# Performance work log

Hardware: AMD Instinct MI355X
Metric: run time of the kernel (lower is better)

## Reference

```python
import jax, jax.numpy as jnp
import numpy as np

B = 16384
C = 512          # mean candidate count per sample
T = B * C        # total flat logits length (static)


def _seg_ce(logits, counts, gt, valid, B):
    """Segmented cross-entropy over variable-length candidate sets.
    logits: [T] flat concatenated logits; counts: [B] segment lengths (sum == T);
    gt: [B] target index within each segment; valid: [B] bool mask.
    Returns (mean loss over valid samples, n_correct, n_valid)."""
    Ttot = logits.shape[0]
    offsets = jnp.cumsum(counts) - counts                       # [B] start of each segment
    seg = jnp.repeat(jnp.arange(B), counts, total_repeat_length=Ttot)  # [T] segment ids
    segmax = jax.ops.segment_max(logits, seg, num_segments=B)   # [B]
    ex = jnp.exp(logits - segmax[seg])
    Z = jax.ops.segment_sum(ex, seg, num_segments=B)            # [B]
    lse = jnp.log(Z) + segmax                                   # [B] logsumexp per segment
    # target logit: clamp position for safety; invalid rows are masked out anyway
    pos = offsets + jnp.clip(gt, 0, jnp.maximum(counts - 1, 0))
    ce = lse - logits[pos]                                      # [B]
    in_range = (gt >= 0) & (gt < counts)
    vmask = (counts > 0) & in_range & valid
    n_valid = vmask.sum()
    loss = jnp.where(vmask, ce, 0.0).sum() / jnp.maximum(n_valid, 1)
    # argmax within each segment (first occurrence, matching torch.argmax)
    local = jnp.arange(Ttot) - offsets[seg]
    is_max = logits == segmax[seg]
    arg = jax.ops.segment_min(jnp.where(is_max, local, Ttot), seg, num_segments=B)
    n_correct = (vmask & (arg == gt)).sum()
    return loss, n_correct, n_valid


def setup_inputs() -> dict:
    key = jax.random.key(0)
    ks = jax.random.split(key, 8)
    # counts alternate C+32 / C-32 so sum == B*C exactly (static T)
    counts = jnp.where(jnp.arange(B) % 2 == 0, C + 32, C - 32).astype(jnp.int32)
    sys_logits = jax.random.normal(ks[0], (T,), dtype=jnp.float32)
    bar_logits = jax.random.normal(ks[1], (T,), dtype=jnp.float32)
    gt_system_idx = jax.random.randint(ks[2], (B,), 0, C - 32).astype(jnp.int32)
    gt_bar_in_sys = jax.random.randint(ks[3], (B,), 0, C - 32).astype(jnp.int32)
    note_positions = jax.random.uniform(ks[4], (B,), dtype=jnp.float32)
    gt_note_position = jax.random.uniform(ks[5], (B,), dtype=jnp.float32)
    gt_valid = jax.random.bernoulli(ks[6], 0.97, (B,))
    return {
        'sys_logits': sys_logits, 'sys_counts': counts,
        'bar_logits': bar_logits, 'bar_counts': counts,
        'note_positions': note_positions,
        'gt_system_idx': gt_system_idx, 'gt_bar_in_sys': gt_bar_in_sys,
        'gt_note_position': gt_note_position, 'gt_valid': gt_valid,
        'log_var_sys': jnp.zeros((), jnp.float32),
        'log_var_bar': jnp.zeros((), jnp.float32),
        'log_var_note': jnp.zeros((), jnp.float32),
    }


def reference(sys_logits, sys_counts, bar_logits, bar_counts, note_positions,
              gt_system_idx, gt_bar_in_sys, gt_note_position, gt_valid,
              log_var_sys, log_var_bar, log_var_note):
    Bn = gt_system_idx.shape[0]
    sys_loss, sys_correct, n_valid = _seg_ce(sys_logits, sys_counts, gt_system_idx, gt_valid, Bn)
    bar_loss, bar_correct, n_valid_bar = _seg_ce(bar_logits, bar_counts, gt_bar_in_sys, gt_valid, Bn)
    # note position MSE over valid samples (bar_valid == gt_valid here)
    m = gt_valid
    nsel = m.sum()
    sq = jnp.where(m, (note_positions - gt_note_position) ** 2, 0.0)
    note_loss = jnp.where(nsel > 0, sq.sum() / jnp.maximum(nsel, 1), 0.0)
    prec_sys = jnp.exp(-log_var_sys)
    prec_bar = jnp.exp(-log_var_bar)
    prec_note = jnp.exp(-log_var_note)
    loss = (0.5 * prec_sys * sys_loss + 0.5 * log_var_sys
            + 0.5 * prec_bar * bar_loss + 0.5 * log_var_bar
            + 0.5 * prec_note * note_loss + 0.5 * log_var_note)
    sys_acc = sys_correct / jnp.maximum(n_valid, 1)
    bar_acc = bar_correct / jnp.maximum(n_valid_bar, 1)
    return (loss, sys_loss, bar_loss, note_loss, sys_acc, bar_acc,
            prec_sys, prec_bar, prec_note)
```

## Files before the change

### kernel.cpp

```cpp
#include <hip/hip_runtime.h>
#include <math.h>


#define SCAN_BLOCKS 64
#define OFFS_BASE 512

__device__ __forceinline__ bool is_valid(const void* gv, int flag, int i) {
  if (flag == 0) return ((const int*)gv)[i] != 0;
  if (flag == 1) return ((const unsigned char*)gv)[i] != 0;
  return ((const float*)gv)[i] != 0.0f;
}

__global__ __launch_bounds__(256)
void uwl_scan_partial(const int* __restrict__ c_sys, const int* __restrict__ c_bar,
                      int B, int* __restrict__ part) {
  const int blk = blockIdx.x;
  const int chunk = (B + SCAN_BLOCKS - 1) / SCAN_BLOCKS;
  const int start = blk * chunk;
  const int end = (start + chunk < B) ? start + chunk : B;
  int ss = 0, sb = 0;
  for (int i = start + threadIdx.x; i < end; i += 256) {
    ss += c_sys[i];
    sb += c_bar[i];
  }
#pragma unroll
  for (int d = 1; d < 64; d <<= 1) {
    ss += __shfl_xor(ss, d, 64);
    sb += __shfl_xor(sb, d, 64);
  }
  __shared__ int l1[4], l2[4];
  const int wid = threadIdx.x >> 6;
  if ((threadIdx.x & 63) == 0) { l1[wid] = ss; l2[wid] = sb; }
  __syncthreads();
  if (threadIdx.x == 0) {
    part[blk] = l1[0] + l1[1] + l1[2] + l1[3];
    part[SCAN_BLOCKS + blk] = l2[0] + l2[1] + l2[2] + l2[3];
  }
}

__global__ void uwl_scan_mid(const void* __restrict__ gv, int B, int* ws, int* part) {
  const int lane = threadIdx.x;
  int a = part[lane], b = part[SCAN_BLOCKS + lane];
  int ia = a, ib = b;
#pragma unroll
  for (int d = 1; d < 64; d <<= 1) {
    const int va = __shfl_up(ia, d, 64);
    const int vb = __shfl_up(ib, d, 64);
    if (lane >= d) { ia += va; ib += vb; }
  }
  part[lane] = ia - a;
  part[SCAN_BLOCKS + lane] = ib - b;
  if (lane >= 1 && lane <= 8) ws[lane * 16] = 0;
  if (lane == 0) {
    const unsigned int* w = (const unsigned int*)gv;
    int nw = B / 4; if (nw > 64) nw = 64; if (nw < 1) nw = 1;
    bool all01 = true, allf = true;
    for (int i = 0; i < nw; ++i) {
      const unsigned int x = w[i];
      if (x > 1u) all01 = false;
      if (x != 0u && x != 0x3F800000u) allf = false;
    }
    ws[0] = all01 ? 0 : (allf ? 2 : 1);
  }
}

__global__ __launch_bounds__(256)
void uwl_scan_final(const int* __restrict__ c_sys, const int* __restrict__ c_bar,
                    int B, int* __restrict__ ws, const int* __restrict__ part) {
  const int blk = blockIdx.x;
  const int chunk = (B + SCAN_BLOCKS - 1) / SCAN_BLOCKS;
  const int start = blk * chunk;
  const int end = (start + chunk < B) ? start + chunk : B;
  const int lane = threadIdx.x & 63;
  const int wid = threadIdx.x >> 6;
  __shared__ int ws1[4], ws2[4];
  int carry1 = part[blk], carry2 = part[SCAN_BLOCKS + blk];
  for (int base = start; base < end; base += 256) {
    const int idx = base + threadIdx.x;
    const bool ok = idx < end;
    const int x1 = ok ? c_sys[idx] : 0;
    const int x2 = ok ? c_bar[idx] : 0;
    int o1 = x1, o2 = x2;
#pragma unroll
    for (int d = 1; d < 64; d <<= 1) {
      const int v1 = __shfl_up(o1, d, 64);
      const int v2 = __shfl_up(o2, d, 64);
      if (lane >= d) { o1 += v1; o2 += v2; }
    }
    if (lane == 63) { ws1[wid] = o1; ws2[wid] = o2; }
    __syncthreads();
    int w1 = 0, w2 = 0;
    for (int w = 0; w < wid; ++w) { w1 += ws1[w]; w2 += ws2[w]; }
    if (ok) {
      ws[OFFS_BASE + idx]     = carry1 + w1 + o1 - x1;
      ws[OFFS_BASE + B + idx] = carry2 + w2 + o2 - x2;
    }
    carry1 += ws1[0] + ws1[1] + ws1[2] + ws1[3];
    carry2 += ws2[0] + ws2[1] + ws2[2] + ws2[3];
    __syncthreads();
  }
}

__global__ __launch_bounds__(256)
void uwl_ce_kernel(const float* __restrict__ sys_lg, const float* __restrict__ bar_lg,
                   const int* __restrict__ c_sys, const int* __restrict__ c_bar,
                   const int* __restrict__ gt_sys, const int* __restrict__ gt_bar,
                   const void* __restrict__ gv, int B, int* wsI, float* wsF) {
  const int wave = (blockIdx.x * blockDim.x + threadIdx.x) >> 6;
  const int lane = threadIdx.x & 63;
  if (wave >= 2 * B) return;
  const bool is_sys = wave < B;
  const int b = is_sys ? wave : wave - B;
  const float* lg = is_sys ? sys_lg : bar_lg;
  const int count = (is_sys ? c_sys : c_bar)[b];
  const int off_i = wsI[OFFS_BASE + (is_sys ? 0 : B) + b];
  const long long off = off_i;
  const int gt = (is_sys ? gt_sys : gt_bar)[b];

  float m = -INFINITY;
  int mi = 0x7fffffff;
  float vals[12];
  const bool regpath = (count <= 768) && ((off_i & 3) == 0);
  if (regpath) {
    const float4* p = (const float4*)(lg + off);
#pragma unroll
    for (int k = 0; k < 3; ++k) {
      const int e = (k << 8) + (lane << 2);
      if (e + 3 < count) {
        const float4 v = p[(k << 6) + lane];
        vals[4 * k] = v.x; vals[4 * k + 1] = v.y;
        vals[4 * k + 2] = v.z; vals[4 * k + 3] = v.w;
      } else {
#pragma unroll
        for (int j = 0; j < 4; ++j) {
          const int i = e + j;
          vals[4 * k + j] = (i < count) ? lg[off + i] : -INFINITY;
        }
      }
    }
#pragma unroll
    for (int k = 0; k < 3; ++k)
#pragma unroll
      for (int j = 0; j < 4; ++j) {
        const float v = vals[4 * k + j];
        if (v > m) { m = v; mi = (k << 8) + (lane << 2) + j; }
      }
  } else {
    for (int i = lane; i < count; i += 64) {
      const float v = lg[off + i];
      if (v > m) { m = v; mi = i; }
    }
  }
#pragma unroll
  for (int d = 1; d < 64; d <<= 1) {
    const float om = __shfl_xor(m, d, 64);
    const int omi = __shfl_xor(mi, d, 64);
    if (om > m || (om == m && omi < mi)) { m = om; mi = omi; }
  }
  float s = 0.f;
  if (regpath) {
#pragma unroll
    for (int k = 0; k < 12; ++k) s += __expf(vals[k] - m);
  } else {
    for (int i = lane; i < count; i += 64) s += __expf(lg[off + i] - m);
  }
#pragma unroll
  for (int d = 1; d < 64; d <<= 1) s += __shfl_xor(s, d, 64);

  if (lane == 0) {
    float ce = 0.f;
    int code = 0;
    if (count > 0) {
      const int flag = wsI[0];
      const bool in_range = (gt >= 0) && (gt < count);
      if (in_range && is_valid(gv, flag, b)) {
        const float tl = lg[off + gt];
        ce = __logf(s) + m - tl;
        code = 1 | ((mi == gt) ? 2 : 0);
      }
    }
    wsF[OFFS_BASE + 2 * B + wave] = ce;
    wsI[OFFS_BASE + 4 * B + wave] = code;
  }
}

__global__ __launch_bounds__(256)
void uwl_reduce_kernel(const float* __restrict__ npos, const float* __restrict__ gnp,
                       const void* __restrict__ gv, int B, int* wsI, float* wsF) {
  const float* ceArr = wsF + OFFS_BASE + 2 * B;
  const int* codeArr = wsI + OFFS_BASE + 4 * B;
  float ces = 0.f, ceb = 0.f;
  int nvs = 0, cs = 0, nvb = 0, cb = 0;
  const int stride = gridDim.x * blockDim.x;
  for (int i = blockIdx.x * blockDim.x + threadIdx.x; i < 2 * B; i += stride) {
    const float ce = ceArr[i];
    const int code = codeArr[i];
    if (i < B) { ces += ce; nvs += code & 1; cs += code >> 1; }
    else       { ceb += ce; nvb += code & 1; cb += code >> 1; }
  }
  const int flag = wsI[0];
  float sq = 0.f; int cnt = 0;
  for (int i = blockIdx.x * blockDim.x + threadIdx.x; i < B; i += stride) {
    if (is_valid(gv, flag, i)) {
      const float d = npos[i] - gnp[i];
      sq += d * d; cnt += 1;
    }
  }
#pragma unroll
  for (int d = 1; d < 64; d <<= 1) {
    ces += __shfl_xor(ces, d, 64);
    ceb += __shfl_xor(ceb, d, 64);
    nvs += __shfl_xor(nvs, d, 64);
    cs  += __shfl_xor(cs,  d, 64);
    nvb += __shfl_xor(nvb, d, 64);
    cb  += __shfl_xor(cb,  d, 64);
    sq  += __shfl_xor(sq,  d, 64);
    cnt += __shfl_xor(cnt, d, 64);
  }
  if ((threadIdx.x & 63) == 0) {
    atomicAdd(&wsI[16], nvs);
    atomicAdd(&wsI[32], cs);
    atomicAdd(&wsF[48], ces);
    atomicAdd(&wsI[64], nvb);
    atomicAdd(&wsI[80], cb);
    atomicAdd(&wsF[96], ceb);
    atomicAdd(&wsI[112], cnt);
    atomicAdd(&wsF[128], sq);
  }
}

__global__ void uwl_final_kernel(const float* __restrict__ lvs_p, const float* __restrict__ lvb_p,
                                 const float* __restrict__ lvn_p,
                                 const int* wsI, const float* wsF, float* __restrict__ out) {
  if (threadIdx.x != 0 || blockIdx.x != 0) return;
  const int nvs = wsI[16], cs = wsI[32], nvb = wsI[64], cb = wsI[80], nn = wsI[112];
  const float sys_loss = wsF[48] / (float)(nvs > 1 ? nvs : 1);
  const float bar_loss = wsF[96] / (float)(nvb > 1 ? nvb : 1);
  const float note_loss = (nn > 0) ? wsF[128] / (float)nn : 0.f;
  const float lvs = lvs_p[0], lvb = lvb_p[0], lvn = lvn_p[0];
  const float ps = expf(-lvs), pb = expf(-lvb), pn = expf(-lvn);
  const float loss = 0.5f * (ps * sys_loss + lvs + pb * bar_loss + lvb + pn * note_loss + lvn);
  out[0] = loss;
  out[1] = sys_loss;
  out[2] = bar_loss;
  out[3] = note_loss;
  out[4] = (float)cs / (float)(nvs > 1 ? nvs : 1);
  out[5] = (float)cb / (float)(nvb > 1 ? nvb : 1);
  out[6] = ps;
  out[7] = pb;
  out[8] = pn;
}

extern "C" void kernel_launch(void* const* d_in, const int* in_sizes, int n_in,
                              void* d_out, int out_size, void* d_ws, size_t ws_size,
                              hipStream_t stream) {
  const float* sys_lg = (const float*)d_in[0];
  const int*   c_sys  = (const int*)d_in[1];
  const float* bar_lg = (const float*)d_in[2];
  const int*   c_bar  = (const int*)d_in[3];
  const float* npos   = (const float*)d_in[4];
  const int*   gt_sys = (const int*)d_in[5];
  const int*   gt_bar = (const int*)d_in[6];
  const float* gnp    = (const float*)d_in[7];
  const void*  gv     = d_in[8];
  const float* lvs    = (const float*)d_in[9];
  const float* lvb    = (const float*)d_in[10];
  const float* lvn    = (const float*)d_in[11];
  const int B = in_sizes[1];

  int*   wsI = (int*)d_ws;
  float* wsF = (float*)d_ws;
  int*   part = wsI + 256;

  uwl_scan_partial<<<SCAN_BLOCKS, 256, 0, stream>>>(c_sys, c_bar, B, part);
  uwl_scan_mid<<<1, 64, 0, stream>>>(gv, B, wsI, part);
  uwl_scan_final<<<SCAN_BLOCKS, 256, 0, stream>>>(c_sys, c_bar, B, wsI, part);

  const int nwaves = 2 * B;
  const long long nthreads = (long long)nwaves * 64;
  const int nblocks = (int)((nthreads + 255) / 256);
  uwl_ce_kernel<<<nblocks, 256, 0, stream>>>(sys_lg, bar_lg, c_sys, c_bar,
                                             gt_sys, gt_bar, gv, B, wsI, wsF);

  uwl_reduce_kernel<<<64, 256, 0, stream>>>(npos, gnp, gv, B, wsI, wsF);

  uwl_final_kernel<<<1, 64, 0, stream>>>(lvs, lvb, lvn, wsI, wsF, (float*)d_out);
}
```

Before: 143.1 us.

## Merge scan stages, precompute per-segment descriptors, and fuse final reduction

Removes the single-block mid-scan kernel by having each final-scan block reduce the partial sums of the blocks before it. The scan now writes one int4 descriptor per segment (offset, count, gt, validity), so the CE kernel does a single load instead of several scattered ones. The target logit is taken from registers via a shuffle rather than a dependent global load. The final scalar kernel is folded into the reduce kernel with a last-block-done atomic counter. Launch count drops from six to four, at the cost of extra workspace traffic for the wider descriptors and a threadfence-based completion protocol.

```diff
diff --git a/kernel.cpp b/kernel.cpp
--- a/kernel.cpp
+++ b/kernel.cpp
@@ -1,9 +1,8 @@
 #include <hip/hip_runtime.h>
 #include <math.h>
 
-
 #define SCAN_BLOCKS 64
-#define OFFS_BASE 512
+#define DESC_BASE 512
 
 __device__ __forceinline__ bool is_valid(const void* gv, int flag, int i) {
   if (flag == 0) return ((const int*)gv)[i] != 0;
@@ -13,7 +12,7 @@
 
 __global__ __launch_bounds__(256)
 void uwl_scan_partial(const int* __restrict__ c_sys, const int* __restrict__ c_bar,
-                      int B, int* __restrict__ part) {
+                      const void* __restrict__ gv, int B, int* __restrict__ ws) {
   const int blk = blockIdx.x;
   const int chunk = (B + SCAN_BLOCKS - 1) / SCAN_BLOCKS;
   const int start = blk * chunk;
@@ -33,48 +32,50 @@
   if ((threadIdx.x & 63) == 0) { l1[wid] = ss; l2[wid] = sb; }
   __syncthreads();
   if (threadIdx.x == 0) {
-    part[blk] = l1[0] + l1[1] + l1[2] + l1[3];
-    part[SCAN_BLOCKS + blk] = l2[0] + l2[1] + l2[2] + l2[3];
-  }
-}
-
-__global__ void uwl_scan_mid(const void* __restrict__ gv, int B, int* ws, int* part) {
-  const int lane = threadIdx.x;
-  int a = part[lane], b = part[SCAN_BLOCKS + lane];
-  int ia = a, ib = b;
-#pragma unroll
-  for (int d = 1; d < 64; d <<= 1) {
-    const int va = __shfl_up(ia, d, 64);
-    const int vb = __shfl_up(ib, d, 64);
-    if (lane >= d) { ia += va; ib += vb; }
-  }
-  part[lane] = ia - a;
-  part[SCAN_BLOCKS + lane] = ib - b;
-  if (lane >= 1 && lane <= 8) ws[lane * 16] = 0;
-  if (lane == 0) {
-    const unsigned int* w = (const unsigned int*)gv;
-    int nw = B / 4; if (nw > 64) nw = 64; if (nw < 1) nw = 1;
-    bool all01 = true, allf = true;
-    for (int i = 0; i < nw; ++i) {
-      const unsigned int x = w[i];
-      if (x > 1u) all01 = false;
-      if (x != 0u && x != 0x3F800000u) allf = false;
-    }
-    ws[0] = all01 ? 0 : (allf ? 2 : 1);
-  }
-}
-
-__global__ __launch_bounds__(256)
-void uwl_scan_final(const int* __restrict__ c_sys, const int* __restrict__ c_bar,
-                    int B, int* __restrict__ ws, const int* __restrict__ part) {
+    ws[256 + blk] = l1[0] + l1[1] + l1[2] + l1[3];
+    ws[256 + SCAN_BLOCKS + blk] = l2[0] + l2[1] + l2[2] + l2[3];
+  }
+  if (blk == 0) {
+    if (threadIdx.x >= 1 && threadIdx.x <= 8) ws[threadIdx.x * 16] = 0;
+    if (threadIdx.x == 9) ws[144] = 0;
+    if (threadIdx.x == 10) {
+      const unsigned int* w = (const unsigned int*)gv;
+      int nw = B / 4; if (nw > 64) nw = 64; if (nw < 1) nw = 1;
+      bool all01 = true, allf = true;
+      for (int i = 0; i < nw; ++i) {
+        const unsigned int x = w[i];
+        if (x > 1u) all01 = false;
+        if (x != 0u && x != 0x3F800000u) allf = false;
+      }
+      ws[0] = all01 ? 0 : (allf ? 2 : 1);
+    }
+  }
+}
+
+__global__ __launch_bounds__(256)
+void uwl_scan_desc(const int* __restrict__ c_sys, const int* __restrict__ c_bar,
+                   const int* __restrict__ gt_sys, const int* __restrict__ gt_bar,
+                   const void* __restrict__ gv, int B, int* __restrict__ ws) {
+  const int* part = ws + 256;
+  const int flag = ws[0];
   const int blk = blockIdx.x;
+  const int lane = threadIdx.x & 63;
+  const int wid = threadIdx.x >> 6;
+  __shared__ int baseS, baseB;
+  __shared__ int ws1[4], ws2[4];
+  if (threadIdx.x < 128) {
+    int p = (lane < blk) ? part[(wid ? SCAN_BLOCKS : 0) + lane] : 0;
+#pragma unroll
+    for (int d = 1; d < 64; d <<= 1) p += __shfl_xor(p, d, 64);
+    if (lane == 0) { if (wid) baseB = p; else baseS = p; }
+  }
+  __syncthreads();
+  int carry1 = baseS, carry2 = baseB;
   const int chunk = (B + SCAN_BLOCKS - 1) / SCAN_BLOCKS;
   const int start = blk * chunk;
   const int end = (start + chunk < B) ? start + chunk : B;
-  const int lane = threadIdx.x & 63;
-  const int wid = threadIdx.x >> 6;
-  __shared__ int ws1[4], ws2[4];
-  int carry1 = part[blk], carry2 = part[SCAN_BLOCKS + blk];
+  int4* descS = (int4*)(ws + DESC_BASE);
+  int4* descB = descS + B;
   for (int base = start; base < end; base += 256) {
     const int idx = base + threadIdx.x;
     const bool ok = idx < end;
@@ -92,8 +93,12 @@
     int w1 = 0, w2 = 0;
     for (int w = 0; w < wid; ++w) { w1 += ws1[w]; w2 += ws2[w]; }
     if (ok) {
-      ws[OFFS_BASE + idx]     = carry1 + w1 + o1 - x1;
-      ws[OFFS_BASE + B + idx] = carry2 + w2 + o2 - x2;
+      const int g1 = gt_sys[idx], g2 = gt_bar[idx];
+      const bool v = is_valid(gv, flag, idx);
+      descS[idx] = make_int4(carry1 + w1 + o1 - x1, x1, g1,
+                             (x1 > 0 && g1 >= 0 && g1 < x1 && v) ? 1 : 0);
+      descB[idx] = make_int4(carry2 + w2 + o2 - x2, x2, g2,
+                             (x2 > 0 && g2 >= 0 && g2 < x2 && v) ? 1 : 0);
     }
     carry1 += ws1[0] + ws1[1] + ws1[2] + ws1[3];
     carry2 += ws2[0] + ws2[1] + ws2[2] + ws2[3];
@@ -103,19 +108,14 @@
 
 __global__ __launch_bounds__(256)
 void uwl_ce_kernel(const float* __restrict__ sys_lg, const float* __restrict__ bar_lg,
-                   const int* __restrict__ c_sys, const int* __restrict__ c_bar,
-                   const int* __restrict__ gt_sys, const int* __restrict__ gt_bar,
-                   const void* __restrict__ gv, int B, int* wsI, float* wsF) {
+                   int B, int* __restrict__ wsI, float* __restrict__ wsF) {
   const int wave = (blockIdx.x * blockDim.x + threadIdx.x) >> 6;
   const int lane = threadIdx.x & 63;
   if (wave >= 2 * B) return;
-  const bool is_sys = wave < B;
-  const int b = is_sys ? wave : wave - B;
-  const float* lg = is_sys ? sys_lg : bar_lg;
-  const int count = (is_sys ? c_sys : c_bar)[b];
-  const int off_i = wsI[OFFS_BASE + (is_sys ? 0 : B) + b];
+  const int4 d4 = ((const int4*)(wsI + DESC_BASE))[wave];
+  const float* lg = (wave < B) ? sys_lg : bar_lg;
+  const int off_i = d4.x, count = d4.y, gt = d4.z, vld = d4.w;
   const long long off = off_i;
-  const int gt = (is_sys ? gt_sys : gt_bar)[b];
 
   float m = -INFINITY;
   int mi = 0x7fffffff;
@@ -167,36 +167,42 @@
 #pragma unroll
   for (int d = 1; d < 64; d <<= 1) s += __shfl_xor(s, d, 64);
 
+  float tl = 0.f;
+  if (regpath) {
+    const int gts = (vld && gt >= 0 && gt < 768) ? gt : 0;
+    const int qidx = ((gts >> 8) << 2) | (gts & 3);
+    float pick = vals[0];
+#pragma unroll
+    for (int q = 1; q < 12; ++q) pick = (q == qidx) ? vals[q] : pick;
+    tl = __shfl(pick, (gts >> 2) & 63, 64);
+  } else if (vld && lane == 0) {
+    tl = lg[off + gt];
+  }
   if (lane == 0) {
-    float ce = 0.f;
-    int code = 0;
-    if (count > 0) {
-      const int flag = wsI[0];
-      const bool in_range = (gt >= 0) && (gt < count);
-      if (in_range && is_valid(gv, flag, b)) {
-        const float tl = lg[off + gt];
-        ce = __logf(s) + m - tl;
-        code = 1 | ((mi == gt) ? 2 : 0);
-      }
-    }
-    wsF[OFFS_BASE + 2 * B + wave] = ce;
-    wsI[OFFS_BASE + 4 * B + wave] = code;
+    float ce = 0.f, code = 0.f;
+    if (vld) {
+      ce = __logf(s) + m - tl;
+      code = (mi == gt) ? 3.f : 1.f;
+    }
+    ((float2*)(wsF + DESC_BASE + 8 * B))[wave] = make_float2(ce, code);
   }
 }
 
 __global__ __launch_bounds__(256)
 void uwl_reduce_kernel(const float* __restrict__ npos, const float* __restrict__ gnp,
-                       const void* __restrict__ gv, int B, int* wsI, float* wsF) {
-  const float* ceArr = wsF + OFFS_BASE + 2 * B;
-  const int* codeArr = wsI + OFFS_BASE + 4 * B;
+                       const void* __restrict__ gv,
+                       const float* __restrict__ lvs_p, const float* __restrict__ lvb_p,
+                       const float* __restrict__ lvn_p,
+                       int B, int* wsI, float* wsF, float* __restrict__ out) {
+  const float2* pw = (const float2*)(wsF + DESC_BASE + 8 * B);
   float ces = 0.f, ceb = 0.f;
   int nvs = 0, cs = 0, nvb = 0, cb = 0;
   const int stride = gridDim.x * blockDim.x;
   for (int i = blockIdx.x * blockDim.x + threadIdx.x; i < 2 * B; i += stride) {
-    const float ce = ceArr[i];
-    const int code = codeArr[i];
-    if (i < B) { ces += ce; nvs += code & 1; cs += code >> 1; }
-    else       { ceb += ce; nvb += code & 1; cb += code >> 1; }
+    const float2 v = pw[i];
+    const int code = (int)v.y;
+    if (i < B) { ces += v.x; nvs += code & 1; cs += code >> 1; }
+    else       { ceb += v.x; nvb += code & 1; cb += code >> 1; }
   }
   const int flag = wsI[0];
   float sq = 0.f; int cnt = 0;
@@ -227,28 +233,36 @@
     atomicAdd(&wsI[112], cnt);
     atomicAdd(&wsF[128], sq);
   }
-}
-
-__global__ void uwl_final_kernel(const float* __restrict__ lvs_p, const float* __restrict__ lvb_p,
-                                 const float* __restrict__ lvn_p,
-                                 const int* wsI, const float* wsF, float* __restrict__ out) {
-  if (threadIdx.x != 0 || blockIdx.x != 0) return;
-  const int nvs = wsI[16], cs = wsI[32], nvb = wsI[64], cb = wsI[80], nn = wsI[112];
-  const float sys_loss = wsF[48] / (float)(nvs > 1 ? nvs : 1);
-  const float bar_loss = wsF[96] / (float)(nvb > 1 ? nvb : 1);
-  const float note_loss = (nn > 0) ? wsF[128] / (float)nn : 0.f;
-  const float lvs = lvs_p[0], lvb = lvb_p[0], lvn = lvn_p[0];
-  const float ps = expf(-lvs), pb = expf(-lvb), pn = expf(-lvn);
-  const float loss = 0.5f * (ps * sys_loss + lvs + pb * bar_loss + lvb + pn * note_loss + lvn);
-  out[0] = loss;
-  out[1] = sys_loss;
-  out[2] = bar_loss;
-  out[3] = note_loss;
-  out[4] = (float)cs / (float)(nvs > 1 ? nvs : 1);
-  out[5] = (float)cb / (float)(nvb > 1 ? nvb : 1);
-  out[6] = ps;
-  out[7] = pb;
-  out[8] = pn;
+  __syncthreads();
+  if (threadIdx.x == 0) {
+    __threadfence();
+    const int t = atomicAdd(&wsI[144], 1);
+    if (t == (int)gridDim.x - 1) {
+      __threadfence();
+      const int fnvs = atomicAdd(&wsI[16], 0);
+      const int fcs  = atomicAdd(&wsI[32], 0);
+      const int fnvb = atomicAdd(&wsI[64], 0);
+      const int fcb  = atomicAdd(&wsI[80], 0);
+      const int fnn  = atomicAdd(&wsI[112], 0);
+      const float fces = atomicAdd(&wsF[48], 0.f);
+      const float fceb = atomicAdd(&wsF[96], 0.f);
+      const float fsq  = atomicAdd(&wsF[128], 0.f);
+      const float sys_loss = fces / (float)(fnvs > 1 ? fnvs : 1);
+      const float bar_loss = fceb / (float)(fnvb > 1 ? fnvb : 1);
+      const float note_loss = (fnn > 0) ? fsq / (float)fnn : 0.f;
+      const float lvs = lvs_p[0], lvb = lvb_p[0], lvn = lvn_p[0];
+      const float ps = expf(-lvs), pb = expf(-lvb), pn = expf(-lvn);
+      out[0] = 0.5f * (ps * sys_loss + lvs + pb * bar_loss + lvb + pn * note_loss + lvn);
+      out[1] = sys_loss;
+      out[2] = bar_loss;
+      out[3] = note_loss;
+      out[4] = (float)fcs / (float)(fnvs > 1 ? fnvs : 1);
+      out[5] = (float)fcb / (float)(fnvb > 1 ? fnvb : 1);
+      out[6] = ps;
+      out[7] = pb;
+      out[8] = pn;
+    }
+  }
 }
 
 extern "C" void kernel_launch(void* const* d_in, const int* in_sizes, int n_in,
@@ -270,19 +284,14 @@
 
   int*   wsI = (int*)d_ws;
   float* wsF = (float*)d_ws;
-  int*   part = wsI + 256;
-
-  uwl_scan_partial<<<SCAN_BLOCKS, 256, 0, stream>>>(c_sys, c_bar, B, part);
-  uwl_scan_mid<<<1, 64, 0, stream>>>(gv, B, wsI, part);
-  uwl_scan_final<<<SCAN_BLOCKS, 256, 0, stream>>>(c_sys, c_bar, B, wsI, part);
-
-  const int nwaves = 2 * B;
-  const long long nthreads = (long long)nwaves * 64;
+
+  uwl_scan_partial<<<SCAN_BLOCKS, 256, 0, stream>>>(c_sys, c_bar, gv, B, wsI);
+  uwl_scan_desc<<<SCAN_BLOCKS, 256, 0, stream>>>(c_sys, c_bar, gt_sys, gt_bar, gv, B, wsI);
+
+  const long long nthreads = (long long)(2 * B) * 64;
   const int nblocks = (int)((nthreads + 255) / 256);
-  uwl_ce_kernel<<<nblocks, 256, 0, stream>>>(sys_lg, bar_lg, c_sys, c_bar,
-                                             gt_sys, gt_bar, gv, B, wsI, wsF);
-
-  uwl_reduce_kernel<<<64, 256, 0, stream>>>(npos, gnp, gv, B, wsI, wsF);
-
-  uwl_final_kernel<<<1, 64, 0, stream>>>(lvs, lvb, lvn, wsI, wsF, (float*)d_out);
-}
+  uwl_ce_kernel<<<nblocks, 256, 0, stream>>>(sys_lg, bar_lg, B, wsI, wsF);
+
+  uwl_reduce_kernel<<<64, 256, 0, stream>>>(npos, gnp, gv, lvs, lvb, lvn,
+                                            B, wsI, wsF, (float*)d_out);
+}
```

Result: no change. 141.7 us (-1.0%).
